# Kernel optimization log

Hardware: AMD Instinct MI355X
Metric: run time of the kernel (lower is better)

The kernel has to match this reference:

```python
import jax, jax.numpy as jnp
import numpy as np

HID, FFN, NE, TOPK = 1024, 4096, 8, 2


def setup_inputs() -> dict:
    key = jax.random.key(0)
    ks = jax.random.split(key, 4)
    x = jax.random.normal(ks[0], (2, 2048, HID), dtype=jnp.float32)
    # router: nn.Linear(hidden, num_experts, bias=False), init std=0.02; stored as [H, E]
    Wr = jax.random.normal(ks[1], (HID, NE), dtype=jnp.float32) * 0.02
    # per-expert FFN weights stacked on leading expert axis
    W1 = jax.random.normal(ks[2], (NE, HID, FFN), dtype=jnp.float32) * (1.0 / np.sqrt(HID))
    b1 = jnp.zeros((NE, FFN), dtype=jnp.float32)
    W2 = jax.random.normal(ks[3], (NE, FFN, HID), dtype=jnp.float32) * (1.0 / np.sqrt(FFN))
    b2 = jnp.zeros((NE, HID), dtype=jnp.float32)
    return {"x": x, "Wr": Wr, "W1": W1, "b1": b1, "W2": W2, "b2": b2}


def reference(x, Wr, W1, b1, W2, b2):
    B, S, H = x.shape
    E = Wr.shape[1]
    T = B * S
    xf = x.reshape(T, H)                                  # [T, H]
    logits = xf @ Wr                                      # [T, E]
    probs = jax.nn.softmax(logits, axis=-1)
    topk_p, topk_i = jax.lax.top_k(probs, TOPK)           # [T, K]
    topk_p = topk_p / jnp.sum(topk_p, axis=-1, keepdims=True)
    # dense combine weights: c[t, e] = normalized prob if expert e selected for token t else 0
    c = jnp.zeros((T, E), dtype=xf.dtype).at[jnp.arange(T)[:, None], topk_i].add(topk_p)

    def expert_step(acc, ew):
        w1, bb1, w2, bb2, ce = ew                         # ce: [T]
        h = jax.nn.gelu(xf @ w1 + bb1, approximate=False)  # exact GELU like nn.GELU()
        y = h @ w2 + bb2                                  # [T, H]
        return acc + ce[:, None] * y, None

    out, _ = jax.lax.scan(expert_step, jnp.zeros_like(xf), (W1, b1, W2, b2, c.T))
    return out.reshape(B, S, H)
```

## Files before the change

### kernel.cpp

```cpp
#include <hip/hip_runtime.h>
#include <hip/hip_bf16.h>

#define H 1024
#define F 4096
#define NE 8
#define T 4096
#define KSPLIT2 2

typedef unsigned short u16;
typedef float floatx4 __attribute__((ext_vector_type(4)));
typedef short short8 __attribute__((ext_vector_type(8)));

__device__ __forceinline__ u16 f2bf(float f) {
  union { float f; unsigned int u; } c; c.f = f;
  unsigned int u = c.u;
  return (u16)((u + 0x7fffu + ((u >> 16) & 1u)) >> 16);
}

__device__ __forceinline__ void load16_lds(const u16* g, u16* l) {
  __builtin_amdgcn_global_load_lds(
      (const __attribute__((address_space(1))) unsigned int*)g,
      (__attribute__((address_space(3))) unsigned int*)l, 16, 0, 0);
}

__device__ __forceinline__ float gelu_f(float v) {
  float y = fabsf(v) * 0.70710678118f;
  float t = __builtin_amdgcn_rcpf(fmaf(0.3275911f, y, 1.0f));
  float p = t * fmaf(t, fmaf(t, fmaf(t, fmaf(t, 1.061405429f, -1.453152027f),
                                     1.421413741f), -0.284496736f), 0.254829592f);
  float e = __builtin_amdgcn_exp2f(-y * y * 1.44269504f);
  float erfv = fmaf(-p, e, 1.0f);
  return fmaf(0.5f * fabsf(v), erfv, 0.5f * v);
}

__global__ __launch_bounds__(256) void router_kernel(
    const float* __restrict__ x, const float* __restrict__ Wr,
    int* __restrict__ cnt, int* __restrict__ tok, float* __restrict__ wgt) {
  int t = (blockIdx.x * 256 + threadIdx.x) >> 6;
  int lane = threadIdx.x & 63;
  const float* xr = x + (size_t)t * H;
  double p[NE];
#pragma unroll
  for (int e = 0; e < NE; ++e) p[e] = 0.0;
  for (int k = lane; k < H; k += 64) {
    float xv = xr[k];
    const float4* wr4 = reinterpret_cast<const float4*>(Wr + k * NE);
    float4 a = wr4[0], b = wr4[1];
    p[0] += (double)xv * a.x; p[1] += (double)xv * a.y;
    p[2] += (double)xv * a.z; p[3] += (double)xv * a.w;
    p[4] += (double)xv * b.x; p[5] += (double)xv * b.y;
    p[6] += (double)xv * b.z; p[7] += (double)xv * b.w;
  }
#pragma unroll
  for (int e = 0; e < NE; ++e) {
#pragma unroll
    for (int off = 32; off; off >>= 1) p[e] += __shfl_down(p[e], off, 64);
  }
  if (lane == 0) {
    int i0 = 0;
#pragma unroll
    for (int e = 1; e < NE; ++e) if (p[e] > p[i0]) i0 = e;
    int i1 = (i0 == 0) ? 1 : 0;
#pragma unroll
    for (int e = 0; e < NE; ++e) if (e != i0 && p[e] > p[i1]) i1 = e;
    double d = exp(p[i1] - p[i0]);
    float w0 = (float)(1.0 / (1.0 + d));
    float w1 = (float)(d / (1.0 + d));
    int pos0 = atomicAdd(&cnt[i0], 1);
    tok[i0 * T + pos0] = t; wgt[i0 * T + pos0] = w0;
    int pos1 = atomicAdd(&cnt[i1], 1);
    tok[i1 * T + pos1] = t; wgt[i1 * T + pos1] = w1;
  }
}

__global__ void offsets_kernel(const int* __restrict__ cnt, int* __restrict__ off) {
  if (threadIdx.x == 0) {
    int s = 0;
#pragma unroll
    for (int e = 0; e < NE; ++e) { off[e] = s; s += cnt[e]; }
    off[NE] = s;
  }
}

__global__ __launch_bounds__(256) void convert_x_kernel(
    const float* __restrict__ x, u16* __restrict__ xb) {
  int i = blockIdx.x * 256 + threadIdx.x;
  float4 v = reinterpret_cast<const float4*>(x)[i];
  ushort4 o;
  o.x = f2bf(v.x); o.y = f2bf(v.y); o.z = f2bf(v.z); o.w = f2bf(v.w);
  reinterpret_cast<ushort4*>(xb)[i] = o;
}

__global__ __launch_bounds__(256) void transpose_both_kernel(
    const float* __restrict__ W1, const float* __restrict__ W2,
    u16* __restrict__ W1t, u16* __restrict__ W2t) {
  __shared__ u16 tile[64][72];
  int z = blockIdx.z;
  int e = z & 7;
  const float* s; u16* d; int R, C, c0, r0;
  if (z < NE) {
    s = W1 + (size_t)e * H * F; d = W1t + (size_t)e * H * F;
    R = H; C = F; c0 = blockIdx.x << 6; r0 = blockIdx.y << 6;
  } else {
    s = W2 + (size_t)e * F * H; d = W2t + (size_t)e * F * H;
    R = F; C = H; c0 = blockIdx.y << 6; r0 = blockIdx.x << 6;
  }
  int t = threadIdx.x;
  int rl = t >> 4, cl = (t & 15) << 2;
#pragma unroll
  for (int i = 0; i < 4; ++i) {
    float4 v = *reinterpret_cast<const float4*>(&s[(size_t)(r0 + rl + i * 16) * C + c0 + cl]);
    ushort4 o; o.x = f2bf(v.x); o.y = f2bf(v.y); o.z = f2bf(v.z); o.w = f2bf(v.w);
    *reinterpret_cast<ushort4*>(&tile[rl + i * 16][cl]) = o;
  }
  __syncthreads();
  int cl2 = t >> 4, rl2 = (t & 15) << 2;
#pragma unroll
  for (int i = 0; i < 4; ++i) {
    ushort4 o;
    o.x = tile[rl2 + 0][cl2 + i * 16];
    o.y = tile[rl2 + 1][cl2 + i * 16];
    o.z = tile[rl2 + 2][cl2 + i * 16];
    o.w = tile[rl2 + 3][cl2 + i * 16];
    *reinterpret_cast<ushort4*>(&d[(size_t)(c0 + cl2 + i * 16) * R + r0 + rl2]) = o;
  }
}

__global__ __launch_bounds__(256) void gemm1_kernel(
    const u16* __restrict__ Xb, const u16* __restrict__ W1t,
    const float* __restrict__ b1, const int* __restrict__ cnt,
    const int* __restrict__ off, const int* __restrict__ tok,
    u16* __restrict__ Hc) {
  int e = blockIdx.z;
  int n = cnt[e];
  int m0 = blockIdx.y << 7;
  if (m0 >= n) return;
  int n0 = blockIdx.x << 7;
  int rb = off[e];

  __shared__ alignas(16) u16 As[2][128 * 32];
  __shared__ alignas(16) u16 Bs[2][128 * 32];
  __shared__ int tokS[128];

  int tid = threadIdx.x;
  if (tid < 128) {
    int s = m0 + tid;
    tokS[tid] = (s < n) ? tok[e * T + s] : 0;
  }
  __syncthreads();

  int kchunk = (((tid & 3) ^ ((tid >> 3) & 3))) * 8;
  const u16* W1e = W1t + (size_t)e * F * H;
  const u16* aP0 = Xb + (size_t)tokS[tid >> 2] * H + kchunk;
  const u16* aP1 = Xb + (size_t)tokS[64 + (tid >> 2)] * H + kchunk;
  const u16* bP0 = W1e + (size_t)(n0 + (tid >> 2)) * H + kchunk;
  const u16* bP1 = W1e + (size_t)(n0 + 64 + (tid >> 2)) * H + kchunk;

  int wv = tid >> 6, lane = tid & 63;
  int wm = wv >> 1, wn = wv & 1;
  int quad = lane >> 4, l16 = lane & 15;

  floatx4 acc[4][4];
#pragma unroll
  for (int mt = 0; mt < 4; ++mt)
#pragma unroll
    for (int nt = 0; nt < 4; ++nt) acc[mt][nt] = floatx4{0.f, 0.f, 0.f, 0.f};

  int qa = (quad ^ ((l16 >> 1) & 3)) * 8;
  int aOff[4], bOff[4];
#pragma unroll
  for (int i = 0; i < 4; ++i) {
    aOff[i] = (wm * 64 + i * 16 + l16) * 32 + qa;
    bOff[i] = (wn * 64 + i * 16 + l16) * 32 + qa;
  }

#define STAGE1(buf, kk)                                   \
  do {                                                    \
    load16_lds(aP0 + (kk), &As[buf][tid * 8]);            \
    load16_lds(aP1 + (kk), &As[buf][(tid + 256) * 8]);    \
    load16_lds(bP0 + (kk), &Bs[buf][tid * 8]);            \
    load16_lds(bP1 + (kk), &Bs[buf][(tid + 256) * 8]);    \
  } while (0)

  const int NIT = H / 32;
  STAGE1(0, 0);
  STAGE1(1, 32);
  for (int it = 0; it < NIT; ++it) {
    if (it >= NIT - 1) asm volatile("s_waitcnt vmcnt(0)" ::: "memory");
    else               asm volatile("s_waitcnt vmcnt(4)" ::: "memory");
    __builtin_amdgcn_s_barrier();
    int cur = it & 1;
    short8 av[4], bv[4];
#pragma unroll
    for (int i = 0; i < 4; ++i) {
      av[i] = *reinterpret_cast<const short8*>(&As[cur][aOff[i]]);
      bv[i] = *reinterpret_cast<const short8*>(&Bs[cur][bOff[i]]);
    }
#pragma unroll
    for (int mt = 0; mt < 4; ++mt)
#pragma unroll
      for (int nt = 0; nt < 4; ++nt)
        acc[mt][nt] = __builtin_amdgcn_mfma_f32_16x16x32_bf16(av[mt], bv[nt], acc[mt][nt], 0, 0, 0);
    __builtin_amdgcn_s_barrier();
    if (it + 2 < NIT) STAGE1(cur, (it + 2) * 32);
  }
#undef STAGE1

  float b1v[4];
#pragma unroll
  for (int nt = 0; nt < 4; ++nt)
    b1v[nt] = b1[e * F + n0 + wn * 64 + nt * 16 + l16];
#pragma unroll
  for (int mt = 0; mt < 4; ++mt) {
#pragma unroll
    for (int i = 0; i < 4; ++i) {
      int row = wm * 64 + mt * 16 + quad * 4 + i;
      int gr = m0 + row;
      if (gr < n) {
        u16* hrow = Hc + (size_t)(rb + gr) * F + n0 + wn * 64 + l16;
#pragma unroll
        for (int nt = 0; nt < 4; ++nt) {
          float v = acc[mt][nt][i] + b1v[nt];
          hrow[nt * 16] = f2bf(gelu_f(v));
        }
      }
    }
  }
}

__global__ __launch_bounds__(256) void gemm2_kernel(
    const u16* __restrict__ Hc, const u16* __restrict__ W2t,
    const float* __restrict__ b2, const int* __restrict__ cnt,
    const int* __restrict__ off, const int* __restrict__ tok,
    const float* __restrict__ wgt, float* __restrict__ out) {
  int e = blockIdx.z >> 1;
  int kc = blockIdx.z & 1;
  int n = cnt[e];
  int m0 = blockIdx.y << 7;
  if (m0 >= n) return;
  int n0 = blockIdx.x << 7;
  int rb = off[e];

  __shared__ alignas(16) u16 As[2][128 * 32];
  __shared__ alignas(16) u16 Bs[2][128 * 32];

  int tid = threadIdx.x;
  int kchunk = (((tid & 3) ^ ((tid >> 3) & 3))) * 8;
  const u16* W2e = W2t + (size_t)e * F * H;
  const u16* aP0 = Hc + (size_t)(rb + m0 + (tid >> 2)) * F + kchunk;
  const u16* aP1 = Hc + (size_t)(rb + m0 + 64 + (tid >> 2)) * F + kchunk;
  const u16* bP0 = W2e + (size_t)(n0 + (tid >> 2)) * F + kchunk;
  const u16* bP1 = W2e + (size_t)(n0 + 64 + (tid >> 2)) * F + kchunk;

  int wv = tid >> 6, lane = tid & 63;
  int wm = wv >> 1, wn = wv & 1;
  int quad = lane >> 4, l16 = lane & 15;

  floatx4 acc[4][4];
#pragma unroll
  for (int mt = 0; mt < 4; ++mt)
#pragma unroll
    for (int nt = 0; nt < 4; ++nt) acc[mt][nt] = floatx4{0.f, 0.f, 0.f, 0.f};

  int qa = (quad ^ ((l16 >> 1) & 3)) * 8;
  int aOff[4], bOff[4];
#pragma unroll
  for (int i = 0; i < 4; ++i) {
    aOff[i] = (wm * 64 + i * 16 + l16) * 32 + qa;
    bOff[i] = (wn * 64 + i * 16 + l16) * 32 + qa;
  }

#define STAGE2(buf, kk)                                   \
  do {                                                    \
    load16_lds(aP0 + (kk), &As[buf][tid * 8]);            \
    load16_lds(aP1 + (kk), &As[buf][(tid + 256) * 8]);    \
    load16_lds(bP0 + (kk), &Bs[buf][tid * 8]);            \
    load16_lds(bP1 + (kk), &Bs[buf][(tid + 256) * 8]);    \
  } while (0)

  const int kBeg = kc * (F / KSPLIT2);
  const int NIT = (F / KSPLIT2) / 32;
  STAGE2(0, kBeg);
  STAGE2(1, kBeg + 32);
  for (int it = 0; it < NIT; ++it) {
    if (it >= NIT - 1) asm volatile("s_waitcnt vmcnt(0)" ::: "memory");
    else               asm volatile("s_waitcnt vmcnt(4)" ::: "memory");
    __builtin_amdgcn_s_barrier();
    int cur = it & 1;
    short8 av[4], bv[4];
#pragma unroll
    for (int i = 0; i < 4; ++i) {
      av[i] = *reinterpret_cast<const short8*>(&As[cur][aOff[i]]);
      bv[i] = *reinterpret_cast<const short8*>(&Bs[cur][bOff[i]]);
    }
#pragma unroll
    for (int mt = 0; mt < 4; ++mt)
#pragma unroll
      for (int nt = 0; nt < 4; ++nt)
        acc[mt][nt] = __builtin_amdgcn_mfma_f32_16x16x32_bf16(av[mt], bv[nt], acc[mt][nt], 0, 0, 0);
    __builtin_amdgcn_s_barrier();
    if (it + 2 < NIT) STAGE2(cur, kBeg + (it + 2) * 32);
  }
#undef STAGE2

  float b2v[4];
#pragma unroll
  for (int nt = 0; nt < 4; ++nt)
    b2v[nt] = (kc == 0) ? b2[e * H + n0 + wn * 64 + nt * 16 + l16] : 0.0f;
#pragma unroll
  for (int mt = 0; mt < 4; ++mt) {
#pragma unroll
    for (int i = 0; i < 4; ++i) {
      int row = wm * 64 + mt * 16 + quad * 4 + i;
      int gr = m0 + row;
      if (gr < n) {
        float wv2 = wgt[e * T + gr];
        int tk = tok[e * T + gr];
        float* orow = out + (size_t)tk * H + n0 + wn * 64 + l16;
#pragma unroll
        for (int nt = 0; nt < 4; ++nt)
          atomicAdd(orow + nt * 16, (acc[mt][nt][i] + b2v[nt]) * wv2);
      }
    }
  }
}

extern "C" void kernel_launch(void* const* d_in, const int* in_sizes, int n_in,
                              void* d_out, int out_size, void* d_ws, size_t ws_size,
                              hipStream_t stream) {
  const float* x  = (const float*)d_in[0];
  const float* Wr = (const float*)d_in[1];
  const float* W1 = (const float*)d_in[2];
  const float* b1 = (const float*)d_in[3];
  const float* W2 = (const float*)d_in[4];
  const float* b2 = (const float*)d_in[5];
  float* out = (float*)d_out;

  char* ws = (char*)d_ws;
  int*   cnt = (int*)(ws + 0);
  int*   off = (int*)(ws + 256);
  int*   tok = (int*)(ws + 4096);
  float* wgt = (float*)(ws + 135168);
  u16*   Xb  = (u16*)(ws + 266240);
  u16*   W1t = (u16*)(ws + 8654848);
  u16*   W2t = (u16*)(ws + 75763712);
  u16*   Hc  = (u16*)(ws + 142872576);

  hipMemsetAsync(cnt, 0, 64, stream);
  hipMemsetAsync(out, 0, (size_t)out_size * sizeof(float), stream);

  router_kernel<<<dim3(T / 4), dim3(256), 0, stream>>>(x, Wr, cnt, tok, wgt);
  offsets_kernel<<<dim3(1), dim3(64), 0, stream>>>(cnt, off);
  convert_x_kernel<<<dim3((T * H / 4) / 256), dim3(256), 0, stream>>>(x, Xb);
  transpose_both_kernel<<<dim3(64, 16, 16), dim3(256), 0, stream>>>(W1, W2, W1t, W2t);
  gemm1_kernel<<<dim3(F / 128, 32, NE), dim3(256), 0, stream>>>(Xb, W1t, b1, cnt, off, tok, Hc);
  gemm2_kernel<<<dim3(H / 128, 32, NE * KSPLIT2), dim3(256), 0, stream>>>(Hc, W2t, b2, cnt, off, tok, wgt, out);
}
```

Measured before the change: 676.2 us.

## Merge prep kernels and overlap W2 transpose with expert GEMM1

Router, x conversion and the W1 transpose now run as one launch using block-index ranges. The W2 transpose is interleaved into the GEMM1 grid, so memory-bound transpose blocks can overlap compute-bound MFMA blocks, with the shared memory unioned between the two roles. GEMM2 switches to a flattened 1D grid with expert-fastest ordering, meant to help scheduling and L2 reuse. This removes launch gaps and serialization, but it makes the grid mapping harder to follow and gives the GEMM1 blocks contention from transpose traffic.

```diff
diff --git a/kernel.cpp b/kernel.cpp
--- a/kernel.cpp
+++ b/kernel.cpp
@@ -33,79 +33,9 @@
   return fmaf(0.5f * fabsf(v), erfv, 0.5f * v);
 }
 
-__global__ __launch_bounds__(256) void router_kernel(
-    const float* __restrict__ x, const float* __restrict__ Wr,
-    int* __restrict__ cnt, int* __restrict__ tok, float* __restrict__ wgt) {
-  int t = (blockIdx.x * 256 + threadIdx.x) >> 6;
-  int lane = threadIdx.x & 63;
-  const float* xr = x + (size_t)t * H;
-  double p[NE];
-#pragma unroll
-  for (int e = 0; e < NE; ++e) p[e] = 0.0;
-  for (int k = lane; k < H; k += 64) {
-    float xv = xr[k];
-    const float4* wr4 = reinterpret_cast<const float4*>(Wr + k * NE);
-    float4 a = wr4[0], b = wr4[1];
-    p[0] += (double)xv * a.x; p[1] += (double)xv * a.y;
-    p[2] += (double)xv * a.z; p[3] += (double)xv * a.w;
-    p[4] += (double)xv * b.x; p[5] += (double)xv * b.y;
-    p[6] += (double)xv * b.z; p[7] += (double)xv * b.w;
-  }
-#pragma unroll
-  for (int e = 0; e < NE; ++e) {
-#pragma unroll
-    for (int off = 32; off; off >>= 1) p[e] += __shfl_down(p[e], off, 64);
-  }
-  if (lane == 0) {
-    int i0 = 0;
-#pragma unroll
-    for (int e = 1; e < NE; ++e) if (p[e] > p[i0]) i0 = e;
-    int i1 = (i0 == 0) ? 1 : 0;
-#pragma unroll
-    for (int e = 0; e < NE; ++e) if (e != i0 && p[e] > p[i1]) i1 = e;
-    double d = exp(p[i1] - p[i0]);
-    float w0 = (float)(1.0 / (1.0 + d));
-    float w1 = (float)(d / (1.0 + d));
-    int pos0 = atomicAdd(&cnt[i0], 1);
-    tok[i0 * T + pos0] = t; wgt[i0 * T + pos0] = w0;
-    int pos1 = atomicAdd(&cnt[i1], 1);
-    tok[i1 * T + pos1] = t; wgt[i1 * T + pos1] = w1;
-  }
-}
-
-__global__ void offsets_kernel(const int* __restrict__ cnt, int* __restrict__ off) {
-  if (threadIdx.x == 0) {
-    int s = 0;
-#pragma unroll
-    for (int e = 0; e < NE; ++e) { off[e] = s; s += cnt[e]; }
-    off[NE] = s;
-  }
-}
-
-__global__ __launch_bounds__(256) void convert_x_kernel(
-    const float* __restrict__ x, u16* __restrict__ xb) {
-  int i = blockIdx.x * 256 + threadIdx.x;
-  float4 v = reinterpret_cast<const float4*>(x)[i];
-  ushort4 o;
-  o.x = f2bf(v.x); o.y = f2bf(v.y); o.z = f2bf(v.z); o.w = f2bf(v.w);
-  reinterpret_cast<ushort4*>(xb)[i] = o;
-}
-
-__global__ __launch_bounds__(256) void transpose_both_kernel(
-    const float* __restrict__ W1, const float* __restrict__ W2,
-    u16* __restrict__ W1t, u16* __restrict__ W2t) {
-  __shared__ u16 tile[64][72];
-  int z = blockIdx.z;
-  int e = z & 7;
-  const float* s; u16* d; int R, C, c0, r0;
-  if (z < NE) {
-    s = W1 + (size_t)e * H * F; d = W1t + (size_t)e * H * F;
-    R = H; C = F; c0 = blockIdx.x << 6; r0 = blockIdx.y << 6;
-  } else {
-    s = W2 + (size_t)e * F * H; d = W2t + (size_t)e * F * H;
-    R = F; C = H; c0 = blockIdx.y << 6; r0 = blockIdx.x << 6;
-  }
-  int t = threadIdx.x;
+__device__ __forceinline__ void transpose_tile(
+    const float* __restrict__ s, u16* __restrict__ d, int R, int C,
+    int r0, int c0, u16 (*tile)[72], int t) {
   int rl = t >> 4, cl = (t & 15) << 2;
 #pragma unroll
   for (int i = 0; i < 4; ++i) {
@@ -126,33 +56,124 @@
   }
 }
 
-__global__ __launch_bounds__(256) void gemm1_kernel(
+__global__ __launch_bounds__(256) void prep_kernel(
+    const float* __restrict__ x, const float* __restrict__ Wr,
+    const float* __restrict__ W1,
+    int* __restrict__ cnt, int* __restrict__ tok, float* __restrict__ wgt,
+    u16* __restrict__ xb, u16* __restrict__ W1t) {
+  __shared__ u16 tile[64][72];
+  int bid = blockIdx.x;
+  int tid = threadIdx.x;
+  if (bid < 1024) {
+    int t = (bid * 256 + tid) >> 6;
+    int lane = tid & 63;
+    const float* xr = x + (size_t)t * H;
+    double p[NE];
+#pragma unroll
+    for (int e = 0; e < NE; ++e) p[e] = 0.0;
+    for (int k = lane; k < H; k += 64) {
+      float xv = xr[k];
+      const float4* wr4 = reinterpret_cast<const float4*>(Wr + k * NE);
+      float4 a = wr4[0], b = wr4[1];
+      p[0] += (double)xv * a.x; p[1] += (double)xv * a.y;
+      p[2] += (double)xv * a.z; p[3] += (double)xv * a.w;
+      p[4] += (double)xv * b.x; p[5] += (double)xv * b.y;
+      p[6] += (double)xv * b.z; p[7] += (double)xv * b.w;
+    }
+#pragma unroll
+    for (int e = 0; e < NE; ++e) {
+#pragma unroll
+      for (int off = 32; off; off >>= 1) p[e] += __shfl_down(p[e], off, 64);
+    }
+    if (lane == 0) {
+      int i0 = 0;
+#pragma unroll
+      for (int e = 1; e < NE; ++e) if (p[e] > p[i0]) i0 = e;
+      int i1 = (i0 == 0) ? 1 : 0;
+#pragma unroll
+      for (int e = 0; e < NE; ++e) if (e != i0 && p[e] > p[i1]) i1 = e;
+      double d = exp(p[i1] - p[i0]);
+      float w0 = (float)(1.0 / (1.0 + d));
+      float w1 = (float)(d / (1.0 + d));
+      int pos0 = atomicAdd(&cnt[i0], 1);
+      tok[i0 * T + pos0] = t; wgt[i0 * T + pos0] = w0;
+      int pos1 = atomicAdd(&cnt[i1], 1);
+      tok[i1 * T + pos1] = t; wgt[i1 * T + pos1] = w1;
+    }
+  } else if (bid < 5120) {
+    int i = (bid - 1024) * 256 + tid;
+    float4 v = reinterpret_cast<const float4*>(x)[i];
+    ushort4 o;
+    o.x = f2bf(v.x); o.y = f2bf(v.y); o.z = f2bf(v.z); o.w = f2bf(v.w);
+    reinterpret_cast<ushort4*>(xb)[i] = o;
+  } else {
+    int b = bid - 5120;
+    int e = b >> 10, rem = b & 1023;
+    int c0 = (rem & 63) << 6;
+    int r0 = (rem >> 6) << 6;
+    transpose_tile(W1 + (size_t)e * H * F, W1t + (size_t)e * H * F,
+                   H, F, r0, c0, tile, tid);
+  }
+}
+
+__global__ void offsets_kernel(const int* __restrict__ cnt, int* __restrict__ off) {
+  if (threadIdx.x == 0) {
+    int s = 0;
+#pragma unroll
+    for (int e = 0; e < NE; ++e) { off[e] = s; s += cnt[e]; }
+    off[NE] = s;
+  }
+}
+
+struct SmG {
+  u16 As[2][128 * 32];
+  u16 Bs[2][128 * 32];
+  int tokS[128];
+};
+union SmU {
+  SmG g;
+  u16 tile[64][72];
+};
+
+__global__ __launch_bounds__(256) void gemm1_trw2_kernel(
     const u16* __restrict__ Xb, const u16* __restrict__ W1t,
     const float* __restrict__ b1, const int* __restrict__ cnt,
     const int* __restrict__ off, const int* __restrict__ tok,
-    u16* __restrict__ Hc) {
-  int e = blockIdx.z;
+    u16* __restrict__ Hc,
+    const float* __restrict__ W2, u16* __restrict__ W2t) {
+  __shared__ alignas(16) SmU sm;
+  int bid = blockIdx.x;
+  int tid = threadIdx.x;
+  int grp = bid >> 4, sub = bid & 15;
+
+  if (sub >= 8) {
+    int t = grp * 8 + (sub - 8);
+    int e = t >> 10, rem = t & 1023;
+    int r0 = (rem & 63) << 6;
+    int c0 = (rem >> 6) << 6;
+    transpose_tile(W2 + (size_t)e * F * H, W2t + (size_t)e * F * H,
+                   F, H, r0, c0, (u16(*)[72])sm.tile, tid);
+    return;
+  }
+
+  int e = sub;
+  int by = grp & 31, bx = grp >> 5;
   int n = cnt[e];
-  int m0 = blockIdx.y << 7;
+  int m0 = by << 7;
   if (m0 >= n) return;
-  int n0 = blockIdx.x << 7;
+  int n0 = bx << 7;
   int rb = off[e];
 
-  __shared__ alignas(16) u16 As[2][128 * 32];
-  __shared__ alignas(16) u16 Bs[2][128 * 32];
-  __shared__ int tokS[128];
-
-  int tid = threadIdx.x;
   if (tid < 128) {
     int s = m0 + tid;
-    tokS[tid] = (s < n) ? tok[e * T + s] : 0;
+    sm.g.tokS[tid] = (s < n) ? tok[e * T + s] : 0;
   }
   __syncthreads();
 
   int kchunk = (((tid & 3) ^ ((tid >> 3) & 3))) * 8;
   const u16* W1e = W1t + (size_t)e * F * H;
-  const u16* aP0 = Xb + (size_t)tokS[tid >> 2] * H + kchunk;
-  const u16* aP1 = Xb + (size_t)tokS[64 + (tid >> 2)] * H + kchunk;
+  const u16* aP0 = Xb + (size_t)sm.g.tokS[tid >> 2] * H + kchunk;
+  const u16* aP1 = Xb + (size_t)sm.g.tokS[64 + (tid >> 2)] * H + kchunk;
   const u16* bP0 = W1e + (size_t)(n0 + (tid >> 2)) * H + kchunk;
   const u16* bP1 = W1e + (size_t)(n0 + 64 + (tid >> 2)) * H + kchunk;
 
@@ -174,12 +195,12 @@
     bOff[i] = (wn * 64 + i * 16 + l16) * 32 + qa;
   }
 
-#define STAGE1(buf, kk)                                   \
-  do {                                                    \
-    load16_lds(aP0 + (kk), &As[buf][tid * 8]);            \
-    load16_lds(aP1 + (kk), &As[buf][(tid + 256) * 8]);    \
-    load16_lds(bP0 + (kk), &Bs[buf][tid * 8]);            \
-    load16_lds(bP1 + (kk), &Bs[buf][(tid + 256) * 8]);    \
+#define STAGE1(buf, kk)                                        \
+  do {                                                         \
+    load16_lds(aP0 + (kk), &sm.g.As[buf][tid * 8]);            \
+    load16_lds(aP1 + (kk), &sm.g.As[buf][(tid + 256) * 8]);    \
+    load16_lds(bP0 + (kk), &sm.g.Bs[buf][tid * 8]);            \
+    load16_lds(bP1 + (kk), &sm.g.Bs[buf][(tid + 256) * 8]);    \
   } while (0)
 
   const int NIT = H / 32;
@@ -193,8 +214,8 @@
     short8 av[4], bv[4];
 #pragma unroll
     for (int i = 0; i < 4; ++i) {
-      av[i] = *reinterpret_cast<const short8*>(&As[cur][aOff[i]]);
-      bv[i] = *reinterpret_cast<const short8*>(&Bs[cur][bOff[i]]);
+      av[i] = *reinterpret_cast<const short8*>(&sm.g.As[cur][aOff[i]]);
+      bv[i] = *reinterpret_cast<const short8*>(&sm.g.Bs[cur][bOff[i]]);
     }
 #pragma unroll
     for (int mt = 0; mt < 4; ++mt)
@@ -233,12 +254,16 @@
     const float* __restrict__ b2, const int* __restrict__ cnt,
     const int* __restrict__ off, const int* __restrict__ tok,
     const float* __restrict__ wgt, float* __restrict__ out) {
-  int e = blockIdx.z >> 1;
-  int kc = blockIdx.z & 1;
+  int bid = blockIdx.x;
+  int e = bid & 7;
+  int rem = bid >> 3;
+  int by = rem & 31;
+  int kc = (rem >> 5) & 1;
+  int bx = rem >> 6;
   int n = cnt[e];
-  int m0 = blockIdx.y << 7;
+  int m0 = by << 7;
   if (m0 >= n) return;
-  int n0 = blockIdx.x << 7;
+  int n0 = bx << 7;
   int rb = off[e];
 
   __shared__ alignas(16) u16 As[2][128 * 32];
@@ -349,10 +374,8 @@
   hipMemsetAsync(cnt, 0, 64, stream);
   hipMemsetAsync(out, 0, (size_t)out_size * sizeof(float), stream);
 
-  router_kernel<<<dim3(T / 4), dim3(256), 0, stream>>>(x, Wr, cnt, tok, wgt);
+  prep_kernel<<<dim3(13312), dim3(256), 0, stream>>>(x, Wr, W1, cnt, tok, wgt, Xb, W1t);
   offsets_kernel<<<dim3(1), dim3(64), 0, stream>>>(cnt, off);
-  convert_x_kernel<<<dim3((T * H / 4) / 256), dim3(256), 0, stream>>>(x, Xb);
-  transpose_both_kernel<<<dim3(64, 16, 16), dim3(256), 0, stream>>>(W1, W2, W1t, W2t);
-  gemm1_kernel<<<dim3(F / 128, 32, NE), dim3(256), 0, stream>>>(Xb, W1t, b1, cnt, off, tok, Hc);
-  gemm2_kernel<<<dim3(H / 128, 32, NE * KSPLIT2), dim3(256), 0, stream>>>(Hc, W2t, b2, cnt, off, tok, wgt, out);
-}
+  gemm1_trw2_kernel<<<dim3(16384), dim3(256), 0, stream>>>(Xb, W1t, b1, cnt, off, tok, Hc, W2, W2t);
+  gemm2_kernel<<<dim3(4096), dim3(256), 0, stream>>>(Hc, W2t, b2, cnt, off, tok, wgt, out);
+}
```

After: 707.4 us. 1.05x slower.

## Retile expert GEMMs to 256x256x64 blocks with 512 threads and flattened grid

Applied to the files above, without the earlier changes.

Both expert GEMMs move from 128x128 tiles with a K-step of 32 on 256 threads to 256x256 tiles with a K-step of 64 on 512 threads. The LDS swizzle is reworked for the wider K-chunk, and the 3D grid is flattened into a 1D grid with the expert index in the low bits. The goal is more operand reuse per LDS load and less global traffic per FLOP. In exchange, LDS use grows to about 128KB per block, and `__launch_bounds__(512,2)` with 128 accumulator floats per thread risks register pressure or spills. The row-block count per expert is also capped at 6, so any expert routed more than 1536 tokens would be silently truncated; this assumes a balanced router.

```diff
diff --git a/kernel.cpp b/kernel.cpp
--- a/kernel.cpp
+++ b/kernel.cpp
@@ -126,83 +126,97 @@
   }
 }
 
-__global__ __launch_bounds__(256) void gemm1_kernel(
+
+__global__ __launch_bounds__(512, 2) void gemm1_kernel(
     const u16* __restrict__ Xb, const u16* __restrict__ W1t,
     const float* __restrict__ b1, const int* __restrict__ cnt,
     const int* __restrict__ off, const int* __restrict__ tok,
     u16* __restrict__ Hc) {
-  int e = blockIdx.z;
+  int bid = blockIdx.x;
+  int e = bid & 7;
+  int rem = bid >> 3;
+  int by = rem % 6;
+  int bx = rem / 6;
   int n = cnt[e];
-  int m0 = blockIdx.y << 7;
+  int m0 = by << 8;
   if (m0 >= n) return;
-  int n0 = blockIdx.x << 7;
+  int n0 = bx << 8;
   int rb = off[e];
 
-  __shared__ alignas(16) u16 As[2][128 * 32];
-  __shared__ alignas(16) u16 Bs[2][128 * 32];
-  __shared__ int tokS[128];
+  __shared__ alignas(16) u16 As[2][256 * 64];
+  __shared__ alignas(16) u16 Bs[2][256 * 64];
+  __shared__ int tokS[256];
 
   int tid = threadIdx.x;
-  if (tid < 128) {
+  if (tid < 256) {
     int s = m0 + tid;
     tokS[tid] = (s < n) ? tok[e * T + s] : 0;
   }
   __syncthreads();
 
-  int kchunk = (((tid & 3) ^ ((tid >> 3) & 3))) * 8;
   const u16* W1e = W1t + (size_t)e * F * H;
-  const u16* aP0 = Xb + (size_t)tokS[tid >> 2] * H + kchunk;
-  const u16* aP1 = Xb + (size_t)tokS[64 + (tid >> 2)] * H + kchunk;
-  const u16* bP0 = W1e + (size_t)(n0 + (tid >> 2)) * H + kchunk;
-  const u16* bP1 = W1e + (size_t)(n0 + 64 + (tid >> 2)) * H + kchunk;
+  const u16* aP[4]; const u16* bP[4];
+#pragma unroll
+  for (int s = 0; s < 4; ++s) {
+    int g = tid + s * 512;
+    int r = g >> 3, p = g & 7;
+    int kcc = (p ^ (r & 7)) * 8;
+    aP[s] = Xb + (size_t)tokS[r] * H + kcc;
+    bP[s] = W1e + (size_t)(n0 + r) * H + kcc;
+  }
 
   int wv = tid >> 6, lane = tid & 63;
-  int wm = wv >> 1, wn = wv & 1;
+  int wm = wv >> 2, wn = wv & 3;
   int quad = lane >> 4, l16 = lane & 15;
 
-  floatx4 acc[4][4];
-#pragma unroll
-  for (int mt = 0; mt < 4; ++mt)
+  floatx4 acc[8][4];
+#pragma unroll
+  for (int mt = 0; mt < 8; ++mt)
 #pragma unroll
     for (int nt = 0; nt < 4; ++nt) acc[mt][nt] = floatx4{0.f, 0.f, 0.f, 0.f};
 
-  int qa = (quad ^ ((l16 >> 1) & 3)) * 8;
-  int aOff[4], bOff[4];
-#pragma unroll
-  for (int i = 0; i < 4; ++i) {
-    aOff[i] = (wm * 64 + i * 16 + l16) * 32 + qa;
-    bOff[i] = (wn * 64 + i * 16 + l16) * 32 + qa;
-  }
-
-#define STAGE1(buf, kk)                                   \
-  do {                                                    \
-    load16_lds(aP0 + (kk), &As[buf][tid * 8]);            \
-    load16_lds(aP1 + (kk), &As[buf][(tid + 256) * 8]);    \
-    load16_lds(bP0 + (kk), &Bs[buf][tid * 8]);            \
-    load16_lds(bP1 + (kk), &Bs[buf][(tid + 256) * 8]);    \
+  int xq[2];
+#pragma unroll
+  for (int kk = 0; kk < 2; ++kk) xq[kk] = ((kk * 4 + quad) ^ (l16 & 7)) * 8;
+  int aRow[8], bRow[4];
+#pragma unroll
+  for (int mt = 0; mt < 8; ++mt) aRow[mt] = (wm * 128 + mt * 16 + l16) * 64;
+#pragma unroll
+  for (int nt = 0; nt < 4; ++nt) bRow[nt] = (wn * 64 + nt * 16 + l16) * 64;
+
+#define STAGE1(buf, kk0)                                          \
+  do {                                                            \
+    _Pragma("unroll")                                             \
+    for (int s = 0; s < 4; ++s) {                                 \
+      load16_lds(aP[s] + (kk0), &As[buf][(tid + s * 512) * 8]);   \
+      load16_lds(bP[s] + (kk0), &Bs[buf][(tid + s * 512) * 8]);   \
+    }                                                             \
   } while (0)
 
-  const int NIT = H / 32;
+  const int NIT = H / 64;
   STAGE1(0, 0);
-  STAGE1(1, 32);
+  STAGE1(1, 64);
   for (int it = 0; it < NIT; ++it) {
     if (it >= NIT - 1) asm volatile("s_waitcnt vmcnt(0)" ::: "memory");
-    else               asm volatile("s_waitcnt vmcnt(4)" ::: "memory");
+    else               asm volatile("s_waitcnt vmcnt(8)" ::: "memory");
     __builtin_amdgcn_s_barrier();
     int cur = it & 1;
-    short8 av[4], bv[4];
-#pragma unroll
-    for (int i = 0; i < 4; ++i) {
-      av[i] = *reinterpret_cast<const short8*>(&As[cur][aOff[i]]);
-      bv[i] = *reinterpret_cast<const short8*>(&Bs[cur][bOff[i]]);
+#pragma unroll
+    for (int kk = 0; kk < 2; ++kk) {
+      short8 bv[4];
+#pragma unroll
+      for (int nt = 0; nt < 4; ++nt)
+        bv[nt] = *reinterpret_cast<const short8*>(&Bs[cur][bRow[nt] + xq[kk]]);
+#pragma unroll
+      for (int mt = 0; mt < 8; ++mt) {
+        short8 av = *reinterpret_cast<const short8*>(&As[cur][aRow[mt] + xq[kk]]);
+#pragma unroll
+        for (int nt = 0; nt < 4; ++nt)
+          acc[mt][nt] = __builtin_amdgcn_mfma_f32_16x16x32_bf16(av, bv[nt], acc[mt][nt], 0, 0, 0);
+      }
     }
-#pragma unroll
-    for (int mt = 0; mt < 4; ++mt)
-#pragma unroll
-      for (int nt = 0; nt < 4; ++nt)
-        acc[mt][nt] = __builtin_amdgcn_mfma_f32_16x16x32_bf16(av[mt], bv[nt], acc[mt][nt], 0, 0, 0);
     __builtin_amdgcn_s_barrier();
-    if (it + 2 < NIT) STAGE1(cur, (it + 2) * 32);
+    if (it + 2 < NIT) STAGE1(cur, (it + 2) * 64);
   }
 #undef STAGE1
 
@@ -211,10 +225,10 @@
   for (int nt = 0; nt < 4; ++nt)
     b1v[nt] = b1[e * F + n0 + wn * 64 + nt * 16 + l16];
 #pragma unroll
-  for (int mt = 0; mt < 4; ++mt) {
+  for (int mt = 0; mt < 8; ++mt) {
 #pragma unroll
     for (int i = 0; i < 4; ++i) {
-      int row = wm * 64 + mt * 16 + quad * 4 + i;
+      int row = wm * 128 + mt * 16 + quad * 4 + i;
       int gr = m0 + row;
       if (gr < n) {
         u16* hrow = Hc + (size_t)(rb + gr) * F + n0 + wn * 64 + l16;
@@ -228,78 +242,93 @@
   }
 }
 
-__global__ __launch_bounds__(256) void gemm2_kernel(
+__global__ __launch_bounds__(512, 2) void gemm2_kernel(
     const u16* __restrict__ Hc, const u16* __restrict__ W2t,
     const float* __restrict__ b2, const int* __restrict__ cnt,
     const int* __restrict__ off, const int* __restrict__ tok,
     const float* __restrict__ wgt, float* __restrict__ out) {
-  int e = blockIdx.z >> 1;
-  int kc = blockIdx.z & 1;
+  int bid = blockIdx.x;
+  int e = bid & 7;
+  int rem = bid >> 3;
+  int by = rem % 6;
+  int rem2 = rem / 6;
+  int kc = rem2 & 1;
+  int bx = rem2 >> 1;
   int n = cnt[e];
-  int m0 = blockIdx.y << 7;
+  int m0 = by << 8;
   if (m0 >= n) return;
-  int n0 = blockIdx.x << 7;
+  int n0 = bx << 8;
   int rb = off[e];
 
-  __shared__ alignas(16) u16 As[2][128 * 32];
-  __shared__ alignas(16) u16 Bs[2][128 * 32];
+  __shared__ alignas(16) u16 As[2][256 * 64];
+  __shared__ alignas(16) u16 Bs[2][256 * 64];
 
   int tid = threadIdx.x;
-  int kchunk = (((tid & 3) ^ ((tid >> 3) & 3))) * 8;
   const u16* W2e = W2t + (size_t)e * F * H;
-  const u16* aP0 = Hc + (size_t)(rb + m0 + (tid >> 2)) * F + kchunk;
-  const u16* aP1 = Hc + (size_t)(rb + m0 + 64 + (tid >> 2)) * F + kchunk;
-  const u16* bP0 = W2e + (size_t)(n0 + (tid >> 2)) * F + kchunk;
-  const u16* bP1 = W2e + (size_t)(n0 + 64 + (tid >> 2)) * F + kchunk;
+  const u16* aP[4]; const u16* bP[4];
+#pragma unroll
+  for (int s = 0; s < 4; ++s) {
+    int g = tid + s * 512;
+    int r = g >> 3, p = g & 7;
+    int kcc = (p ^ (r & 7)) * 8;
+    int r2 = m0 + r; if (r2 > n - 1) r2 = n - 1;
+    aP[s] = Hc + (size_t)(rb + r2) * F + kcc;
+    bP[s] = W2e + (size_t)(n0 + r) * F + kcc;
+  }
 
   int wv = tid >> 6, lane = tid & 63;
-  int wm = wv >> 1, wn = wv & 1;
+  int wm = wv >> 2, wn = wv & 3;
   int quad = lane >> 4, l16 = lane & 15;
 
-  floatx4 acc[4][4];
-#pragma unroll
-  for (int mt = 0; mt < 4; ++mt)
+  floatx4 acc[8][4];
+#pragma unroll
+  for (int mt = 0; mt < 8; ++mt)
 #pragma unroll
     for (int nt = 0; nt < 4; ++nt) acc[mt][nt] = floatx4{0.f, 0.f, 0.f, 0.f};
 
-  int qa = (quad ^ ((l16 >> 1) & 3)) * 8;
-  int aOff[4], bOff[4];
-#pragma unroll
-  for (int i = 0; i < 4; ++i) {
-    aOff[i] = (wm * 64 + i * 16 + l16) * 32 + qa;
-    bOff[i] = (wn * 64 + i * 16 + l16) * 32 + qa;
-  }
-
-#define STAGE2(buf, kk)                                   \
-  do {                                                    \
-    load16_lds(aP0 + (kk), &As[buf][tid * 8]);            \
-    load16_lds(aP1 + (kk), &As[buf][(tid + 256) * 8]);    \
-    load16_lds(bP0 + (kk), &Bs[buf][tid * 8]);            \
-    load16_lds(bP1 + (kk), &Bs[buf][(tid + 256) * 8]);    \
+  int xq[2];
+#pragma unroll
+  for (int kk = 0; kk < 2; ++kk) xq[kk] = ((kk * 4 + quad) ^ (l16 & 7)) * 8;
+  int aRow[8], bRow[4];
+#pragma unroll
+  for (int mt = 0; mt < 8; ++mt) aRow[mt] = (wm * 128 + mt * 16 + l16) * 64;
+#pragma unroll
+  for (int nt = 0; nt < 4; ++nt) bRow[nt] = (wn * 64 + nt * 16 + l16) * 64;
+
+#define STAGE2(buf, kk0)                                          \
+  do {                                                            \
+    _Pragma("unroll")                                             \
+    for (int s = 0; s < 4; ++s) {                                 \
+      load16_lds(aP[s] + (kk0), &As[buf][(tid + s * 512) * 8]);   \
+      load16_lds(bP[s] + (kk0), &Bs[buf][(tid + s * 512) * 8]);   \
+    }                                                             \
   } while (0)
 
   const int kBeg = kc * (F / KSPLIT2);
-  const int NIT = (F / KSPLIT2) / 32;
+  const int NIT = (F / KSPLIT2) / 64;
   STAGE2(0, kBeg);
-  STAGE2(1, kBeg + 32);
+  STAGE2(1, kBeg + 64);
   for (int it = 0; it < NIT; ++it) {
     if (it >= NIT - 1) asm volatile("s_waitcnt vmcnt(0)" ::: "memory");
-    else               asm volatile("s_waitcnt vmcnt(4)" ::: "memory");
+    else               asm volatile("s_waitcnt vmcnt(8)" ::: "memory");
     __builtin_amdgcn_s_barrier();
     int cur = it & 1;
-    short8 av[4], bv[4];
-#pragma unroll
-    for (int i = 0; i < 4; ++i) {
-      av[i] = *reinterpret_cast<const short8*>(&As[cur][aOff[i]]);
-      bv[i] = *reinterpret_cast<const short8*>(&Bs[cur][bOff[i]]);
+#pragma unroll
+    for (int kk = 0; kk < 2; ++kk) {
+      short8 bv[4];
+#pragma unroll
+      for (int nt = 0; nt < 4; ++nt)
+        bv[nt] = *reinterpret_cast<const short8*>(&Bs[cur][bRow[nt] + xq[kk]]);
+#pragma unroll
+      for (int mt = 0; mt < 8; ++mt) {
+        short8 av = *reinterpret_cast<const short8*>(&As[cur][aRow[mt] + xq[kk]]);
+#pragma unroll
+        for (int nt = 0; nt < 4; ++nt)
+          acc[mt][nt] = __builtin_amdgcn_mfma_f32_16x16x32_bf16(av, bv[nt], acc[mt][nt], 0, 0, 0);
+      }
     }
-#pragma unroll
-    for (int mt = 0; mt < 4; ++mt)
-#pragma unroll
-      for (int nt = 0; nt < 4; ++nt)
-        acc[mt][nt] = __builtin_amdgcn_mfma_f32_16x16x32_bf16(av[mt], bv[nt], acc[mt][nt], 0, 0, 0);
     __builtin_amdgcn_s_barrier();
-    if (it + 2 < NIT) STAGE2(cur, kBeg + (it + 2) * 32);
+    if (it + 2 < NIT) STAGE2(cur, kBeg + (it + 2) * 64);
   }
 #undef STAGE2
 
@@ -308,10 +337,10 @@
   for (int nt = 0; nt < 4; ++nt)
     b2v[nt] = (kc == 0) ? b2[e * H + n0 + wn * 64 + nt * 16 + l16] : 0.0f;
 #pragma unroll
-  for (int mt = 0; mt < 4; ++mt) {
+  for (int mt = 0; mt < 8; ++mt) {
 #pragma unroll
     for (int i = 0; i < 4; ++i) {
-      int row = wm * 64 + mt * 16 + quad * 4 + i;
+      int row = wm * 128 + mt * 16 + quad * 4 + i;
       int gr = m0 + row;
       if (gr < n) {
         float wv2 = wgt[e * T + gr];
@@ -353,6 +382,6 @@
   offsets_kernel<<<dim3(1), dim3(64), 0, stream>>>(cnt, off);
   convert_x_kernel<<<dim3((T * H / 4) / 256), dim3(256), 0, stream>>>(x, Xb);
   transpose_both_kernel<<<dim3(64, 16, 16), dim3(256), 0, stream>>>(W1, W2, W1t, W2t);
-  gemm1_kernel<<<dim3(F / 128, 32, NE), dim3(256), 0, stream>>>(Xb, W1t, b1, cnt, off, tok, Hc);
-  gemm2_kernel<<<dim3(H / 128, 32, NE * KSPLIT2), dim3(256), 0, stream>>>(Hc, W2t, b2, cnt, off, tok, wgt, out);
-}
+  gemm1_kernel<<<dim3(8 * 6 * 16), dim3(512), 0, stream>>>(Xb, W1t, b1, cnt, off, tok, Hc);
+  gemm2_kernel<<<dim3(8 * 6 * 4 * KSPLIT2), dim3(512), 0, stream>>>(Hc, W2t, b2, cnt, off, tok, wgt, out);
+}
```

Result: slower. 726.1 us (+7.4%).

## Replace split-K atomic combine with per-slot buffer and deterministic combine kernel

Applied to the files above, without the earlier changes.

Each token's second routing slot is tagged in its token index. gemm2 drops split-K and atomics and writes weighted expert outputs into a per-token, per-slot buffer, which a new combine kernel sums into the output. gemm2 now runs on a flattened 1D grid with the expert as the fastest-varying index. The transpose kernel writes 16-byte vectors through a re-padded LDS tile. This removes the output memset and global float atomics, at the cost of an extra kernel, a 32 MB intermediate write and read, and half as many gemm2 blocks, each with a longer K loop. The buffer reuses the W1t workspace, which is safe only because gemm1 has finished.

```diff
diff --git a/kernel.cpp b/kernel.cpp
--- a/kernel.cpp
+++ b/kernel.cpp
@@ -5,7 +5,6 @@
 #define F 4096
 #define NE 8
 #define T 4096
-#define KSPLIT2 2
 
 typedef unsigned short u16;
 typedef float floatx4 __attribute__((ext_vector_type(4)));
@@ -67,9 +66,11 @@
     float w0 = (float)(1.0 / (1.0 + d));
     float w1 = (float)(d / (1.0 + d));
     int pos0 = atomicAdd(&cnt[i0], 1);
-    tok[i0 * T + pos0] = t; wgt[i0 * T + pos0] = w0;
+    tok[i0 * T + pos0] = t;
+    wgt[i0 * T + pos0] = w0;
     int pos1 = atomicAdd(&cnt[i1], 1);
-    tok[i1 * T + pos1] = t; wgt[i1 * T + pos1] = w1;
+    tok[i1 * T + pos1] = t | 4096;
+    wgt[i1 * T + pos1] = w1;
   }
 }
 
@@ -94,7 +95,7 @@
 __global__ __launch_bounds__(256) void transpose_both_kernel(
     const float* __restrict__ W1, const float* __restrict__ W2,
     u16* __restrict__ W1t, u16* __restrict__ W2t) {
-  __shared__ u16 tile[64][72];
+  __shared__ u16 tile[64][76];
   int z = blockIdx.z;
   int e = z & 7;
   const float* s; u16* d; int R, C, c0, r0;
@@ -114,15 +115,14 @@
     *reinterpret_cast<ushort4*>(&tile[rl + i * 16][cl]) = o;
   }
   __syncthreads();
-  int cl2 = t >> 4, rl2 = (t & 15) << 2;
-#pragma unroll
-  for (int i = 0; i < 4; ++i) {
-    ushort4 o;
-    o.x = tile[rl2 + 0][cl2 + i * 16];
-    o.y = tile[rl2 + 1][cl2 + i * 16];
-    o.z = tile[rl2 + 2][cl2 + i * 16];
-    o.w = tile[rl2 + 3][cl2 + i * 16];
-    *reinterpret_cast<ushort4*>(&d[(size_t)(c0 + cl2 + i * 16) * R + r0 + rl2]) = o;
+  int cw = t >> 3, rw = (t & 7) << 3;
+#pragma unroll
+  for (int i = 0; i < 2; ++i) {
+    int c = cw + i * 32;
+    short8 o;
+#pragma unroll
+    for (int j = 0; j < 8; ++j) o[j] = (short)tile[rw + j][c];
+    *reinterpret_cast<short8*>(&d[(size_t)(c0 + c) * R + r0 + rw]) = o;
   }
 }
 
@@ -145,7 +145,7 @@
   int tid = threadIdx.x;
   if (tid < 128) {
     int s = m0 + tid;
-    tokS[tid] = (s < n) ? tok[e * T + s] : 0;
+    tokS[tid] = (s < n) ? (tok[e * T + s] & 4095) : 0;
   }
   __syncthreads();
 
@@ -232,13 +232,16 @@
     const u16* __restrict__ Hc, const u16* __restrict__ W2t,
     const float* __restrict__ b2, const int* __restrict__ cnt,
     const int* __restrict__ off, const int* __restrict__ tok,
-    const float* __restrict__ wgt, float* __restrict__ out) {
-  int e = blockIdx.z >> 1;
-  int kc = blockIdx.z & 1;
+    const float* __restrict__ wgt, float* __restrict__ Yb) {
+  int bid = blockIdx.x;
+  int e = bid & 7;
+  int rem = bid >> 3;
+  int by = rem & 31;
+  int bx = rem >> 5;
   int n = cnt[e];
-  int m0 = blockIdx.y << 7;
+  int m0 = by << 7;
   if (m0 >= n) return;
-  int n0 = blockIdx.x << 7;
+  int n0 = bx << 7;
   int rb = off[e];
 
   __shared__ alignas(16) u16 As[2][128 * 32];
@@ -278,10 +281,9 @@
     load16_lds(bP1 + (kk), &Bs[buf][(tid + 256) * 8]);    \
   } while (0)
 
-  const int kBeg = kc * (F / KSPLIT2);
-  const int NIT = (F / KSPLIT2) / 32;
-  STAGE2(0, kBeg);
-  STAGE2(1, kBeg + 32);
+  const int NIT = F / 32;
+  STAGE2(0, 0);
+  STAGE2(1, 32);
   for (int it = 0; it < NIT; ++it) {
     if (it >= NIT - 1) asm volatile("s_waitcnt vmcnt(0)" ::: "memory");
     else               asm volatile("s_waitcnt vmcnt(4)" ::: "memory");
@@ -299,14 +301,14 @@
       for (int nt = 0; nt < 4; ++nt)
         acc[mt][nt] = __builtin_amdgcn_mfma_f32_16x16x32_bf16(av[mt], bv[nt], acc[mt][nt], 0, 0, 0);
     __builtin_amdgcn_s_barrier();
-    if (it + 2 < NIT) STAGE2(cur, kBeg + (it + 2) * 32);
+    if (it + 2 < NIT) STAGE2(cur, (it + 2) * 32);
   }
 #undef STAGE2
 
   float b2v[4];
 #pragma unroll
   for (int nt = 0; nt < 4; ++nt)
-    b2v[nt] = (kc == 0) ? b2[e * H + n0 + wn * 64 + nt * 16 + l16] : 0.0f;
+    b2v[nt] = b2[e * H + n0 + wn * 64 + nt * 16 + l16];
 #pragma unroll
   for (int mt = 0; mt < 4; ++mt) {
 #pragma unroll
@@ -316,13 +318,26 @@
       if (gr < n) {
         float wv2 = wgt[e * T + gr];
         int tk = tok[e * T + gr];
-        float* orow = out + (size_t)tk * H + n0 + wn * 64 + l16;
+        int t2 = tk & 4095, slot = tk >> 12;
+        float* yrow = Yb + ((size_t)t2 * 2 + slot) * H + n0 + wn * 64 + l16;
 #pragma unroll
         for (int nt = 0; nt < 4; ++nt)
-          atomicAdd(orow + nt * 16, (acc[mt][nt][i] + b2v[nt]) * wv2);
+          yrow[nt * 16] = (acc[mt][nt][i] + b2v[nt]) * wv2;
       }
     }
   }
+}
+
+__global__ __launch_bounds__(256) void combine_kernel(
+    const float* __restrict__ Yb, float* __restrict__ out) {
+  int i = blockIdx.x * 256 + threadIdx.x;
+  int t = i >> 8;
+  int h4 = i & 255;
+  const float4* Y4 = reinterpret_cast<const float4*>(Yb);
+  float4 a = Y4[((size_t)t * 2) * 256 + h4];
+  float4 b = Y4[((size_t)t * 2 + 1) * 256 + h4];
+  float4 o; o.x = a.x + b.x; o.y = a.y + b.y; o.z = a.z + b.z; o.w = a.w + b.w;
+  reinterpret_cast<float4*>(out)[i] = o;
 }
 
 extern "C" void kernel_launch(void* const* d_in, const int* in_sizes, int n_in,
@@ -345,14 +360,15 @@
   u16*   W1t = (u16*)(ws + 8654848);
   u16*   W2t = (u16*)(ws + 75763712);
   u16*   Hc  = (u16*)(ws + 142872576);
+  float* Yb  = (float*)(ws + 8654848);
 
   hipMemsetAsync(cnt, 0, 64, stream);
-  hipMemsetAsync(out, 0, (size_t)out_size * sizeof(float), stream);
 
   router_kernel<<<dim3(T / 4), dim3(256), 0, stream>>>(x, Wr, cnt, tok, wgt);
   offsets_kernel<<<dim3(1), dim3(64), 0, stream>>>(cnt, off);
   convert_x_kernel<<<dim3((T * H / 4) / 256), dim3(256), 0, stream>>>(x, Xb);
   transpose_both_kernel<<<dim3(64, 16, 16), dim3(256), 0, stream>>>(W1, W2, W1t, W2t);
   gemm1_kernel<<<dim3(F / 128, 32, NE), dim3(256), 0, stream>>>(Xb, W1t, b1, cnt, off, tok, Hc);
-  gemm2_kernel<<<dim3(H / 128, 32, NE * KSPLIT2), dim3(256), 0, stream>>>(Hc, W2t, b2, cnt, off, tok, wgt, out);
-}
+  gemm2_kernel<<<dim3(2048), dim3(256), 0, stream>>>(Hc, W2t, b2, cnt, off, tok, wgt, Yb);
+  combine_kernel<<<dim3(T * H / 4 / 256), dim3(256), 0, stream>>>(Yb, out);
+}
```

After: 666.1 us. Within noise of the previous version (-1.5%).
